# Kernel optimization log

Hardware: AMD Instinct MI355X
Metric: run time of the kernel (lower is better)

## Reference

```python
import jax, jax.numpy as jnp
import numpy as np

N_NODES = 100000
N_EDGES = 2000000
D = 128
REL_TYPES = 64


def setup_inputs() -> dict:
    key = jax.random.key(0)
    k1, k2, k3, k4 = jax.random.split(key, 4)
    z = jax.random.normal(k1, (N_NODES, D), dtype=jnp.float32)
    edge_index = jax.random.randint(k2, (2, N_EDGES), 0, N_NODES, dtype=jnp.int64)
    rel_id = jax.random.randint(k3, (N_EDGES,), 0, REL_TYPES, dtype=jnp.int64)
    rel = jax.random.normal(k4, (REL_TYPES, D), dtype=jnp.float32)
    return {"z": z, "edge_index": edge_index, "rel_id": rel_id, "rel": rel}


def reference(z, edge_index, rel_id, rel):
    # DistMult: sigmoid(sum_d z[src,d] * rel[rel_id,d] * z[dst,d])
    src = z[edge_index[0]]          # [E, D]
    dst = z[edge_index[1]]          # [E, D]
    r = rel[rel_id]                 # [E, D]
    scores = jnp.sum(src * r * dst, axis=1)  # [E]
    return jax.nn.sigmoid(scores)
```

## Files before the change

kernel.cpp:

```cpp
#include <hip/hip_runtime.h>
#include <hip/hip_fp16.h>
#include <stdint.h>


#define NSRC 8
#define NDST 64
#define NBKT 512
#define NREP 2
#define CNT_STRIDE 16
#define PE 8
#define EPB 128

#if defined(__has_builtin)
#if __has_builtin(__builtin_amdgcn_fdot2)
#define HAS_FDOT2 1
#endif
#endif

typedef _Float16 hv2 __attribute__((ext_vector_type(2)));

__device__ __forceinline__ float dot3_accum(uint32_t a, uint32_t r, uint32_t b,
                                            float acc)
{
#ifdef HAS_FDOT2
    union { uint32_t u; hv2 v; } A, R, B;
    A.u = a; R.u = r; B.u = b;
    const hv2 t = A.v * R.v;
    return __builtin_amdgcn_fdot2(t, B.v, acc, false);
#else
    union { uint32_t u; __half2 h; } A, R, B;
    A.u = a; R.u = r; B.u = b;
    const float2 af = __half22float2(A.h);
    const float2 rf = __half22float2(R.h);
    const float2 bf = __half22float2(B.h);
    acc = fmaf(af.x * rf.x, bf.x, acc);
    acc = fmaf(af.y * rf.y, bf.y, acc);
    return acc;
#endif
}

__device__ __forceinline__ uint32_t bucket_of2(uint32_t s, uint32_t d, uint32_t nn) {
    uint32_t ss = (s * (uint32_t)NSRC) / nn; if (ss > NSRC - 1) ss = NSRC - 1;
    uint32_t ds = (d * (uint32_t)NDST) / nn; if (ds > NDST - 1) ds = NDST - 1;
    return ss * NDST + ds;
}

__device__ __forceinline__ void convert8(const float* __restrict__ x,
                                         __half* __restrict__ xh, int i)
{
    const float4 f0 = ((const float4*)x)[2 * i];
    const float4 f1 = ((const float4*)x)[2 * i + 1];
    union { __half2 h2[4]; uint4 u; } o;
    o.h2[0] = __floats2half2_rn(f0.x, f0.y);
    o.h2[1] = __floats2half2_rn(f0.z, f0.w);
    o.h2[2] = __floats2half2_rn(f1.x, f1.y);
    o.h2[3] = __floats2half2_rn(f1.z, f1.w);
    ((uint4*)xh)[i] = o.u;
}

__global__ __launch_bounds__(256) void aux_merged_kernel(
    const float* __restrict__ z, __half* __restrict__ zh, int n8z,
    const float* __restrict__ rel, __half* __restrict__ rh, int n8r,
    const int* __restrict__ src, const int* __restrict__ dst,
    const int* __restrict__ relid, int E, int nn, int vcap,
    uint32_t* __restrict__ counters, uint64_t* __restrict__ binned,
    int sc_blocks, int zc_blocks)
{
    const int bid = blockIdx.x;
    if (bid >= sc_blocks) {
        const int cb = bid - sc_blocks;
        if (cb < zc_blocks) {
            const int i = cb * 256 + (int)threadIdx.x;
            if (i < n8z) convert8(z, zh, i);
        } else {
            const int i = (cb - zc_blocks) * 256 + (int)threadIdx.x;
            if (i < n8r) convert8(rel, rh, i);
        }
        return;
    }

    __shared__ uint32_t hist[NBKT];
    __shared__ uint32_t cursor[NBKT];

    const int rep = bid & (NREP - 1);
    const int chunk = (E + sc_blocks - 1) / sc_blocks;
    const int lo = bid * chunk;
    const int hi = (lo + chunk < E) ? lo + chunk : E;

    for (int t = threadIdx.x; t < NBKT; t += 256) hist[t] = 0;
    __syncthreads();

    uint64_t pay[PE];
    uint32_t bkt[PE];

    #pragma unroll
    for (int p = 0; p < PE; p++) {
        const int i = lo + p * 256 + (int)threadIdx.x;
        if (i < hi) {
            const uint32_t s = (uint32_t)src[i];
            const uint32_t d = (uint32_t)dst[i];
            const uint32_t r = (uint32_t)relid[i];
            const uint32_t b = bucket_of2(s, d, (uint32_t)nn);
            pay[p] = (uint64_t)s | ((uint64_t)d << 17)
                   | ((uint64_t)r << 34) | ((uint64_t)i << 40);
            bkt[p] = b;
            atomicAdd(&hist[b], 1u);
        } else {
            bkt[p] = 0xFFFFFFFFu;
        }
    }
    __syncthreads();

    for (int t = threadIdx.x; t < NBKT; t += 256) {
        const uint32_t c = hist[t];
        cursor[t] = c ? atomicAdd(&counters[(t * NREP + rep) * CNT_STRIDE], c) : 0u;
    }
    __syncthreads();

    #pragma unroll
    for (int p = 0; p < PE; p++) {
        if (bkt[p] != 0xFFFFFFFFu) {
            const uint32_t pos = atomicAdd(&cursor[bkt[p]], 1u);
            if (pos < (uint32_t)vcap)
                binned[(size_t)(bkt[p] * NREP + rep) * (size_t)vcap + pos] = pay[p];
        }
    }
}

__global__ __launch_bounds__(256) void distmult_bucketed_v4_kernel(
    const __half* __restrict__ zh,
    const uint64_t* __restrict__ binned,
    const uint32_t* __restrict__ counters,
    const __half* __restrict__ relh,
    float* __restrict__ out,
    int vcap, int vcpb)
{
    const int k     = blockIdx.x & 7;
    const int t     = blockIdx.x >> 3;
    const int per_j = NREP * vcpb;
    const int j     = t / per_j;
    const int rem   = t - j * per_j;
    const int rep   = rem / vcpb;
    const int chunk = rem - rep * vcpb;
    const int v     = (k * NDST + j) * NREP + rep;

    uint32_t cnt = counters[v * CNT_STRIDE];
    if (cnt > (uint32_t)vcap) cnt = (uint32_t)vcap;
    const uint32_t el_blk = (uint32_t)chunk * (uint32_t)EPB;
    if (el_blk >= cnt) return;

    __shared__ uint4 rel_lds[1024];
    {
        const uint4* rsrc = (const uint4*)relh;
        #pragma unroll
        for (int q = 0; q < 4; q++)
            rel_lds[threadIdx.x + 256 * q] = rsrc[threadIdx.x + 256 * q];
    }
    __syncthreads();

    const int g    = threadIdx.x >> 3;
    const int lane = threadIdx.x & 7;

    const uint64_t* bb = binned + (size_t)v * (size_t)vcap;
    const uint32_t e_base = el_blk + (uint32_t)g * 4u;

    union U4 { uint4 q; uint32_t w[4]; };
    float acc[4];
    uint32_t eid[4];
    bool valid[4];

    #pragma unroll
    for (int i = 0; i < 4; i++) {
        const uint32_t el = e_base + (uint32_t)i;
        valid[i] = (el < cnt);
        const uint64_t p = bb[valid[i] ? el : 0];
        const uint32_t s = (uint32_t)p & 0x1FFFFu;
        const uint32_t d = (uint32_t)(p >> 17) & 0x1FFFFu;
        const uint32_t r = (uint32_t)(p >> 34) & 0x3Fu;
        eid[i] = (uint32_t)(p >> 40);

        const uint4* sb = (const uint4*)(zh + (size_t)s * 128);
        const uint4* db = (const uint4*)(zh + (size_t)d * 128);
        U4 A0, A1, B0, B1, R0, R1;
        A0.q = sb[lane];
        A1.q = sb[lane + 8];
        B0.q = db[lane];
        B1.q = db[lane + 8];
        R0.q = rel_lds[r * 16 + lane];
        R1.q = rel_lds[r * 16 + lane + 8];

        float a = 0.f;
        #pragma unroll
        for (int q = 0; q < 4; q++) {
            a = dot3_accum(A0.w[q], R0.w[q], B0.w[q], a);
            a = dot3_accum(A1.w[q], R1.w[q], B1.w[q], a);
        }
        acc[i] = a;
    }

    #pragma unroll
    for (int off = 4; off > 0; off >>= 1) {
        #pragma unroll
        for (int i = 0; i < 4; i++)
            acc[i] += __shfl_down(acc[i], off, 8);
    }

    if (lane == 0) {
        #pragma unroll
        for (int i = 0; i < 4; i++)
            if (valid[i])
                out[eid[i]] = 1.0f / (1.0f + __expf(-acc[i]));
    }
}

__global__ __launch_bounds__(256) void convert_kernel(
    const float* __restrict__ x, __half* __restrict__ xh, int n8)
{
    const int i = blockIdx.x * blockDim.x + threadIdx.x;
    if (i < n8) convert8(x, xh, i);
}

__global__ __launch_bounds__(256) void distmult_f16_kernel(
    const __half* __restrict__ zh,
    const int* __restrict__ src_idx, const int* __restrict__ dst_idx,
    const int* __restrict__ rel_id, const __half* __restrict__ relh,
    float* __restrict__ out, int E)
{
    const int gtid = blockIdx.x * blockDim.x + threadIdx.x;
    const int g = gtid >> 4;
    const int lane = threadIdx.x & 15;
    const int e0 = g * 2, e1 = e0 + 1;
    if (e0 >= E) return;
    const bool has1 = (e1 < E);

    const int s0 = src_idx[e0], d0 = dst_idx[e0], r0 = rel_id[e0];
    const int s1 = has1 ? src_idx[e1] : s0;
    const int d1 = has1 ? dst_idx[e1] : d0;
    const int r1 = has1 ? rel_id[e1]  : r0;

    union U4 { uint4 q; uint32_t w[4]; };
    U4 A0, B0, A1, B1, R0, R1;
    A0.q = ((const uint4*)(zh + (size_t)s0 * 128))[lane];
    B0.q = ((const uint4*)(zh + (size_t)d0 * 128))[lane];
    A1.q = ((const uint4*)(zh + (size_t)s1 * 128))[lane];
    B1.q = ((const uint4*)(zh + (size_t)d1 * 128))[lane];
    R0.q = ((const uint4*)(relh + (size_t)r0 * 128))[lane];
    R1.q = ((const uint4*)(relh + (size_t)r1 * 128))[lane];

    float v0 = 0.f, v1 = 0.f;
    #pragma unroll
    for (int q = 0; q < 4; q++) {
        v0 = dot3_accum(A0.w[q], R0.w[q], B0.w[q], v0);
        v1 = dot3_accum(A1.w[q], R1.w[q], B1.w[q], v1);
    }
    #pragma unroll
    for (int off = 8; off > 0; off >>= 1) {
        v0 += __shfl_down(v0, off, 16);
        v1 += __shfl_down(v1, off, 16);
    }
    if (lane == 0) {
        const float o0 = 1.0f / (1.0f + __expf(-v0));
        if (has1) {
            const float o1 = 1.0f / (1.0f + __expf(-v1));
            *((float2*)(out + e0)) = make_float2(o0, o1);
        } else {
            out[e0] = o0;
        }
    }
}

__global__ __launch_bounds__(256) void distmult_f32_kernel(
    const float* __restrict__ z,
    const int* __restrict__ src_idx, const int* __restrict__ dst_idx,
    const int* __restrict__ rel_id, const float* __restrict__ rel,
    float* __restrict__ out, int E)
{
    const int gtid = blockIdx.x * blockDim.x + threadIdx.x;
    const int e = gtid >> 4;
    const int lane = threadIdx.x & 15;
    if (e >= E) return;
    const int s = src_idx[e], d = dst_idx[e], r = rel_id[e];
    const float4* zs = (const float4*)(z + (size_t)s * 128);
    const float4* zd = (const float4*)(z + (size_t)d * 128);
    const float4* rr = (const float4*)(rel + (size_t)r * 128);
    const float4 a0 = zs[lane], a1 = zs[lane + 16];
    const float4 b0 = zd[lane], b1 = zd[lane + 16];
    const float4 c0 = rr[lane], c1 = rr[lane + 16];
    float v = a0.x * c0.x * b0.x + a0.y * c0.y * b0.y
            + a0.z * c0.z * b0.z + a0.w * c0.w * b0.w
            + a1.x * c1.x * b1.x + a1.y * c1.y * b1.y
            + a1.z * c1.z * b1.z + a1.w * c1.w * b1.w;
    #pragma unroll
    for (int off = 8; off > 0; off >>= 1) v += __shfl_down(v, off, 16);
    if (lane == 0) out[e] = 1.0f / (1.0f + __expf(-v));
}

extern "C" void kernel_launch(void* const* d_in, const int* in_sizes, int n_in,
                              void* d_out, int out_size, void* d_ws, size_t ws_size,
                              hipStream_t stream) {
    const float* z     = (const float*)d_in[0];
    const int*   eidx  = (const int*)d_in[1];
    const int*   relid = (const int*)d_in[2];
    const float* rel   = (const float*)d_in[3];
    float*       out   = (float*)d_out;

    const int nz   = in_sizes[0];
    const int E    = in_sizes[2];
    const int nrel = in_sizes[3];
    const int nn   = nz / 128;
    const int* src = eidx;
    const int* dst = eidx + E;

    const int mean_v = E / (NBKT * NREP);
    int vcap = mean_v + E / 16384 + 192;
    vcap = (vcap + EPB - 1) & ~(EPB - 1);
    const int vcpb = vcap / EPB;

    int sc_blocks = (E + PE * 256 - 1) / (PE * 256);
    if (sc_blocks < 1024) sc_blocks = 1024;
    sc_blocks = (sc_blocks + NREP - 1) & ~(NREP - 1);

    const int n8z = nz / 8, n8r = nrel / 8;
    const int zc_blocks = (n8z + 255) / 256;
    const int rc_blocks = (n8r + 255) / 256;

    const size_t sz_zh    = (size_t)nz * sizeof(__half);
    const size_t off_rh   = (sz_zh + 255) & ~(size_t)255;
    const size_t sz_rh    = (size_t)nrel * sizeof(__half);
    const size_t off_cnt  = (off_rh + sz_rh + 255) & ~(size_t)255;
    const size_t sz_cnt   = (size_t)NBKT * NREP * CNT_STRIDE * 4;
    const size_t off_bin  = (off_cnt + sz_cnt + 255) & ~(size_t)255;
    const size_t sz_bin   = (size_t)NBKT * NREP * (size_t)vcap * 8;
    const size_t need     = off_bin + sz_bin;

    const bool rel_ok  = (nrel == 64 * 128);
    const bool bits_ok = (nn <= 131072) && (E <= (1 << 21)) && (nz % 8 == 0);

    if (ws_size >= need && rel_ok && bits_ok) {
        char* ws = (char*)d_ws;
        __half*   zh       = (__half*)(ws);
        __half*   rh       = (__half*)(ws + off_rh);
        uint32_t* counters = (uint32_t*)(ws + off_cnt);
        uint64_t* binned   = (uint64_t*)(ws + off_bin);

        hipMemsetAsync(counters, 0, sz_cnt, stream);
        const int aux_grid = sc_blocks + zc_blocks + rc_blocks;
        aux_merged_kernel<<<aux_grid, 256, 0, stream>>>(
            z, zh, n8z, rel, rh, n8r,
            src, dst, relid, E, nn, vcap, counters, binned,
            sc_blocks, zc_blocks);
        distmult_bucketed_v4_kernel<<<NSRC * NDST * NREP * vcpb, 256, 0, stream>>>(
            zh, binned, counters, rh, out, vcap, vcpb);
    } else if (ws_size >= off_rh + sz_rh && rel_ok && nz % 8 == 0) {
        __half* zh = (__half*)d_ws;
        __half* rh = (__half*)((char*)d_ws + off_rh);
        convert_kernel<<<zc_blocks, 256, 0, stream>>>(z, zh, n8z);
        convert_kernel<<<rc_blocks, 256, 0, stream>>>(rel, rh, n8r);
        const int groups = (E + 1) / 2;
        const int blocks = (groups * 16 + 255) / 256;
        distmult_f16_kernel<<<blocks, 256, 0, stream>>>(
            zh, src, dst, relid, rh, out, E);
    } else {
        const int blocks = (E * 16 + 255) / 256;
        distmult_f32_kernel<<<blocks, 256, 0, stream>>>(z, src, dst, relid, rel, out, E);
    }
}
```

Measured before the change: 216.0 us.

## Vectorize edge index loads per thread and raise bucket replica count

The binning pass now has each thread load 8 contiguous edges through int4 vector reads of src, dst and relid, instead of strided scalar loads. The replica count NREP doubles to 4 to spread atomic contention on the global bucket counters. The minimum number of scatter blocks and the per-bucket capacity formula are also retuned, and chunk is computed on the host rounded to 8. Smaller per-bucket capacity raises the risk of overflow on skewed inputs, and the distmult grid grows with NREP.

```diff
diff --git a/kernel.cpp b/kernel.cpp
--- a/kernel.cpp
+++ b/kernel.cpp
@@ -6,7 +6,7 @@
 #define NSRC 8
 #define NDST 64
 #define NBKT 512
-#define NREP 2
+#define NREP 4
 #define CNT_STRIDE 16
 #define PE 8
 #define EPB 128
@@ -64,7 +64,7 @@
     const int* __restrict__ src, const int* __restrict__ dst,
     const int* __restrict__ relid, int E, int nn, int vcap,
     uint32_t* __restrict__ counters, uint64_t* __restrict__ binned,
-    int sc_blocks, int zc_blocks)
+    int sc_blocks, int zc_blocks, int chunk)
 {
     const int bid = blockIdx.x;
     if (bid >= sc_blocks) {
@@ -83,7 +83,6 @@
     __shared__ uint32_t cursor[NBKT];
 
     const int rep = bid & (NREP - 1);
-    const int chunk = (E + sc_blocks - 1) / sc_blocks;
     const int lo = bid * chunk;
     const int hi = (lo + chunk < E) ? lo + chunk : E;
 
@@ -92,14 +91,33 @@
 
     uint64_t pay[PE];
     uint32_t bkt[PE];
+    int sv[PE], dv[PE], rv[PE];
+
+    const int i0 = lo + (int)threadIdx.x * PE;
+    if (i0 + PE <= E) {
+        *(int4*)&sv[0] = ((const int4*)(src + i0))[0];
+        *(int4*)&sv[4] = ((const int4*)(src + i0))[1];
+        *(int4*)&dv[0] = ((const int4*)(dst + i0))[0];
+        *(int4*)&dv[4] = ((const int4*)(dst + i0))[1];
+        *(int4*)&rv[0] = ((const int4*)(relid + i0))[0];
+        *(int4*)&rv[4] = ((const int4*)(relid + i0))[1];
+    } else {
+        #pragma unroll
+        for (int p = 0; p < PE; p++) {
+            const int i = i0 + p;
+            sv[p] = (i < E) ? src[i] : 0;
+            dv[p] = (i < E) ? dst[i] : 0;
+            rv[p] = (i < E) ? relid[i] : 0;
+        }
+    }
 
     #pragma unroll
     for (int p = 0; p < PE; p++) {
-        const int i = lo + p * 256 + (int)threadIdx.x;
+        const int i = i0 + p;
         if (i < hi) {
-            const uint32_t s = (uint32_t)src[i];
-            const uint32_t d = (uint32_t)dst[i];
-            const uint32_t r = (uint32_t)relid[i];
+            const uint32_t s = (uint32_t)sv[p];
+            const uint32_t d = (uint32_t)dv[p];
+            const uint32_t r = (uint32_t)rv[p];
             const uint32_t b = bucket_of2(s, d, (uint32_t)nn);
             pay[p] = (uint64_t)s | ((uint64_t)d << 17)
                    | ((uint64_t)r << 34) | ((uint64_t)i << 40);
@@ -312,13 +330,14 @@
     const int* dst = eidx + E;
 
     const int mean_v = E / (NBKT * NREP);
-    int vcap = mean_v + E / 16384 + 192;
-    vcap = (vcap + EPB - 1) & ~(EPB - 1);
+    int vcap = (mean_v + 175 + 127) & ~127;
+    if (vcap < 256) vcap = 256;
     const int vcpb = vcap / EPB;
 
     int sc_blocks = (E + PE * 256 - 1) / (PE * 256);
-    if (sc_blocks < 1024) sc_blocks = 1024;
+    if (sc_blocks < 1536) sc_blocks = 1536;
     sc_blocks = (sc_blocks + NREP - 1) & ~(NREP - 1);
+    const int chunk = (((E + sc_blocks - 1) / sc_blocks) + 7) & ~7;
 
     const int n8z = nz / 8, n8r = nrel / 8;
     const int zc_blocks = (n8z + 255) / 256;
@@ -348,7 +367,7 @@
         aux_merged_kernel<<<aux_grid, 256, 0, stream>>>(
             z, zh, n8z, rel, rh, n8r,
             src, dst, relid, E, nn, vcap, counters, binned,
-            sc_blocks, zc_blocks);
+            sc_blocks, zc_blocks, chunk);
         distmult_bucketed_v4_kernel<<<NSRC * NDST * NREP * vcpb, 256, 0, stream>>>(
             zh, binned, counters, rh, out, vcap, vcpb);
     } else if (ws_size >= off_rh + sz_rh && rel_ok && nz % 8 == 0) {
```

Result: slower. 224.8 us (+4.1%).
